# Performance work log

Hardware: AMD Instinct MI355X
Metric: run time of the kernel (lower is better)

Reference implementation:

```python
import jax, jax.numpy as jnp
import numpy as np

D_MODEL = 1024
NUM_HEADS = 16
HEAD_DIM = D_MODEL // NUM_HEADS


def setup_inputs() -> dict:
    key = jax.random.key(0)
    k1, k2, k3 = jax.random.split(key, 3)
    B, T = 4, 2048
    x = jax.random.normal(k1, (B, T, D_MODEL), dtype=jnp.float32)
    # nn.Linear weights: out = x @ W.T; store torch-layout [out_features, in_features]
    w_qkv = jax.random.normal(k2, (3 * D_MODEL, D_MODEL), dtype=jnp.float32) * (D_MODEL ** -0.5)
    w_proj = jax.random.normal(k3, (D_MODEL, D_MODEL), dtype=jnp.float32) * (D_MODEL ** -0.5)
    return {"x": x, "w_qkv": w_qkv, "w_proj": w_proj}


def reference(x, w_qkv, w_proj):
    B, T, C = x.shape
    H, Dh = NUM_HEADS, HEAD_DIM
    qkv = jnp.einsum('btc,fc->btf', x, w_qkv)          # [B,T,3C]
    q, k, v = jnp.split(qkv, 3, axis=2)
    # [B,T,C] -> [B,H,T,Dh]
    q = q.reshape(B, T, H, Dh).transpose(0, 2, 1, 3)
    k = k.reshape(B, T, H, Dh).transpose(0, 2, 1, 3)
    v = v.reshape(B, T, H, Dh).transpose(0, 2, 1, 3)
    scale = Dh ** -0.5
    att = jnp.einsum('bhqd,bhkd->bhqk', q, k) * scale  # [B,H,T,T]
    causal = jnp.tril(jnp.ones((T, T), dtype=bool))
    att = jnp.where(causal, att, -jnp.inf)
    att = jax.nn.softmax(att, axis=-1)
    y = jnp.einsum('bhqk,bhkd->bhqd', att, v)          # [B,H,T,Dh]
    y = y.transpose(0, 2, 1, 3).reshape(B, T, C)
    return jnp.einsum('btc,oc->bto', y, w_proj)
```

## Files before the change

### kernel.cpp

```cpp
#include <hip/hip_runtime.h>
#include <stdint.h>
#include <math.h>

typedef __bf16 bf16;
typedef __bf16 bf16x4 __attribute__((ext_vector_type(4)));
typedef __bf16 bf16x8 __attribute__((ext_vector_type(8)));
typedef float f32x4 __attribute__((ext_vector_type(4)));

#define MFMA16(a, b, c) __builtin_amdgcn_mfma_f32_16x16x32_bf16((a), (b), (c), 0, 0, 0)

typedef __attribute__((address_space(1))) void* as1v;
typedef __attribute__((address_space(3))) void* as3v;

__device__ __forceinline__ void async_ld16(const void* g, void* l) {
  __builtin_amdgcn_global_load_lds((as1v)(uintptr_t)g,
                                   (as3v)(unsigned int)(uintptr_t)l, 16, 0, 0);
}

__global__ __launch_bounds__(256) void cast3_k(const float* __restrict__ x,
                                               const float* __restrict__ wq,
                                               const float* __restrict__ wp,
                                               bf16* __restrict__ xb,
                                               bf16* __restrict__ wqb,
                                               bf16* __restrict__ wpb) {
  const long i = (long)blockIdx.x * 256 + threadIdx.x;
  const float4* src;
  bf16x4* dst;
  long off;
  if (i < 2097152L) {
    src = (const float4*)x;  dst = (bf16x4*)xb;  off = i;
  } else if (i < 2097152L + 786432L) {
    src = (const float4*)wq; dst = (bf16x4*)wqb; off = i - 2097152L;
  } else {
    src = (const float4*)wp; dst = (bf16x4*)wpb; off = i - 2097152L - 786432L;
  }
  float4 v = src[off];
  bf16x4 o;
  o[0] = (bf16)v.x; o[1] = (bf16)v.y; o[2] = (bf16)v.z; o[3] = (bf16)v.w;
  dst[off] = o;
}

__global__ __launch_bounds__(256, 2) void gemm_qkv(const bf16* __restrict__ A,
                                                   const bf16* __restrict__ Bm,
                                                   bf16* __restrict__ qb,
                                                   bf16* __restrict__ kb,
                                                   bf16* __restrict__ vth) {
  __shared__ bf16 As[2][128 * 64];
  __shared__ bf16 Bs[2][192 * 64];
  const int tid  = threadIdx.x;
  const int lane = tid & 63;
  const int wv   = tid >> 6;
  const int wm   = wv >> 1;
  const int wn   = wv & 1;
  const int lr   = lane & 15;
  const int quad = lane >> 4;
  const long m0 = (long)blockIdx.y * 128;
  const long n0 = (long)blockIdx.x * 192;

  const int srow = lane >> 3;
  const int scg  = (lane & 7) ^ srow;
  const int swz  = lr & 7;

  const f32x4 fz = {0.f, 0.f, 0.f, 0.f};
  f32x4 acc[4][6];
#pragma unroll
  for (int i = 0; i < 4; ++i)
#pragma unroll
    for (int j = 0; j < 6; ++j) acc[i][j] = fz;

#define STAGE_QKV(kt, bufi)                                                        \
  do {                                                                             \
    const long kk = (long)(kt) * 64;                                               \
    _Pragma("unroll") for (int i_ = 0; i_ < 4; ++i_)                               \
        async_ld16(&A[(m0 + i_ * 32 + wv * 8 + srow) * 1024 + kk + scg * 8],       \
                   &As[bufi][(i_ * 32 + wv * 8) * 64]);                            \
    _Pragma("unroll") for (int i_ = 0; i_ < 6; ++i_)                               \
        async_ld16(&Bm[(n0 + i_ * 32 + wv * 8 + srow) * 1024 + kk + scg * 8],      \
                   &Bs[bufi][(i_ * 32 + wv * 8) * 64]);                            \
  } while (0)

  STAGE_QKV(0, 0);

#pragma unroll 2
  for (int t = 0; t < 16; ++t) {
    const int cur = t & 1;
    if (t < 15) {
      STAGE_QKV(t + 1, cur ^ 1);
      asm volatile("s_waitcnt vmcnt(10)" ::: "memory");
    } else {
      asm volatile("s_waitcnt vmcnt(0)" ::: "memory");
    }
    __builtin_amdgcn_s_barrier();

    bf16x8 af[2][4], bfr[2][6];
#pragma unroll
    for (int ds = 0; ds < 2; ++ds) {
      const int slot = ((ds << 2) + quad) ^ swz;
#pragma unroll
      for (int mi = 0; mi < 4; ++mi)
        af[ds][mi] = *(const bf16x8*)&As[cur][(wm * 64 + mi * 16 + lr) * 64 + slot * 8];
#pragma unroll
      for (int ni = 0; ni < 6; ++ni)
        bfr[ds][ni] = *(const bf16x8*)&Bs[cur][(wn * 96 + ni * 16 + lr) * 64 + slot * 8];
    }
#pragma unroll
    for (int ds = 0; ds < 2; ++ds)
#pragma unroll
      for (int mi = 0; mi < 4; ++mi)
#pragma unroll
        for (int ni = 0; ni < 6; ++ni)
          acc[mi][ni] = MFMA16(af[ds][mi], bfr[ds][ni], acc[mi][ni]);

    if (t < 15) __builtin_amdgcn_s_barrier();
  }
#undef STAGE_QKV

  const float kS = 0.18033688f;
#pragma unroll
  for (int mi = 0; mi < 4; ++mi) {
    const long row = m0 + wm * 64 + mi * 16 + quad * 4;
#pragma unroll
    for (int ni = 0; ni < 6; ++ni) {
      const long col = n0 + wn * 96 + ni * 16 + lr;
      if (col < 1024) {
#pragma unroll
        for (int r = 0; r < 4; ++r) qb[(row + r) * 1024 + col] = (bf16)(acc[mi][ni][r] * kS);
      } else if (col < 2048) {
        const long kc = col - 1024;
#pragma unroll
        for (int r = 0; r < 4; ++r) kb[(row + r) * 1024 + kc] = (bf16)(acc[mi][ni][r]);
      } else {
        const long vcol = col - 2048;
        const long h = vcol >> 6, d = vcol & 63;
        const long b = row >> 11;
        const long tt = row & 2047;
        bf16x4 pk;
#pragma unroll
        for (int r = 0; r < 4; ++r) pk[r] = (bf16)(acc[mi][ni][r]);
        *(bf16x4*)&vth[(((b << 4) + h) * 64 + d) * 2048 + tt] = pk;
      }
    }
  }
}

__global__ __launch_bounds__(128, 2) void gemm_proj(const bf16* __restrict__ A,
                                                    const bf16* __restrict__ Bm,
                                                    float* __restrict__ C) {
  __shared__ bf16 As[128 * 64];
  __shared__ bf16 Bs[128 * 64];
  const int tid  = threadIdx.x;
  const int lane = tid & 63;
  const int wv   = tid >> 6;
  const int lr   = lane & 15;
  const int quad = lane >> 4;
  const long m0 = (long)blockIdx.y * 128;
  const long n0 = (long)blockIdx.x * 128;

  const int srow = lane >> 3;
  const int scg  = (lane & 7) ^ srow;
  const int swz  = lr & 7;

  const f32x4 fz = {0.f, 0.f, 0.f, 0.f};
  f32x4 acc[4][8];
#pragma unroll
  for (int i = 0; i < 4; ++i)
#pragma unroll
    for (int j = 0; j < 8; ++j) acc[i][j] = fz;

  for (int k0 = 0; k0 < 1024; k0 += 64) {
    __syncthreads();
#pragma unroll
    for (int i = 0; i < 8; ++i) {
      const int rb = wv * 64 + i * 8;
      async_ld16(&A[(m0 + rb + srow) * 1024 + k0 + scg * 8], &As[rb * 64]);
      async_ld16(&Bm[(n0 + rb + srow) * 1024 + k0 + scg * 8], &Bs[rb * 64]);
    }
    __syncthreads();

#pragma unroll
    for (int ds = 0; ds < 2; ++ds) {
      const int slot = ((ds << 2) + quad) ^ swz;
      bf16x8 af[4], bfr[8];
#pragma unroll
      for (int mi = 0; mi < 4; ++mi)
        af[mi] = *(const bf16x8*)&As[(wv * 64 + mi * 16 + lr) * 64 + slot * 8];
#pragma unroll
      for (int ni = 0; ni < 8; ++ni)
        bfr[ni] = *(const bf16x8*)&Bs[(ni * 16 + lr) * 64 + slot * 8];
#pragma unroll
      for (int mi = 0; mi < 4; ++mi)
#pragma unroll
        for (int ni = 0; ni < 8; ++ni)
          acc[mi][ni] = MFMA16(af[mi], bfr[ni], acc[mi][ni]);
    }
  }

#pragma unroll
  for (int mi = 0; mi < 4; ++mi) {
    const long row = m0 + wv * 64 + mi * 16 + quad * 4;
#pragma unroll
    for (int ni = 0; ni < 8; ++ni) {
      const long col = n0 + ni * 16 + lr;
#pragma unroll
      for (int r = 0; r < 4; ++r) C[(row + r) * 1024 + col] = acc[mi][ni][r];
    }
  }
}

__global__ __launch_bounds__(256, 2) void flash_attn5(const bf16* __restrict__ q,
                                                      const bf16* __restrict__ k,
                                                      const bf16* __restrict__ vth,
                                                      bf16* __restrict__ y) {
  __shared__ bf16 Ks[2][64 * 64];
  __shared__ bf16 Vt[64 * 64];
  __shared__ bf16 Ps[4][32 * 72];
  const int tid  = threadIdx.x;
  const int lane = tid & 63;
  const int wv   = tid >> 6;
  const int lr   = lane & 15;
  const int quad = lane >> 4;
  const int p  = blockIdx.x;
  const int bh = blockIdx.y;
  const int b = bh >> 4, h = bh & 15;
  const bf16* qp = q + ((size_t)b * 2048) * 1024 + h * 64;
  const bf16* kp = k + ((size_t)b * 2048) * 1024 + h * 64;
  const bf16* vp = vth + (size_t)bh * 64 * 2048;
  bf16* yp = y + ((size_t)b * 2048) * 1024 + h * 64;

  const int stg_row = lane >> 3;
  const int stg_cg  = (lane & 7) ^ stg_row;
  const int swz     = lr & 7;

  bf16x8 ones;
#pragma unroll
  for (int j = 0; j < 8; ++j) ones[j] = (bf16)1.0f;
  const f32x4 fz = {0.f, 0.f, 0.f, 0.f};

  for (int half = 0; half < 2; ++half) {
    const int qt = half ? p : 15 - p;
    const int q0 = qt * 128;
    const int kb_max = 2 * qt + 1;
    const int kmax_w = 2 * qt + (wv >> 1);

    bf16x8 qf[2][2];
#pragma unroll
    for (int nq = 0; nq < 2; ++nq) {
      const int qrow = q0 + wv * 32 + nq * 16 + lr;
#pragma unroll
      for (int ds = 0; ds < 2; ++ds)
        qf[nq][ds] = *(const bf16x8*)(qp + (size_t)qrow * 1024 + ds * 32 + quad * 8);
    }

    f32x4 o[2][4];
    f32x4 lacc[2];
#pragma unroll
    for (int nq = 0; nq < 2; ++nq) {
      lacc[nq] = fz;
#pragma unroll
      for (int nf = 0; nf < 4; ++nf) o[nq][nf] = fz;
    }

    __syncthreads();
#pragma unroll
    for (int i = 0; i < 2; ++i) {
      const int r = i * 32 + wv * 8 + stg_row;
      async_ld16(kp + (size_t)r * 1024 + stg_cg * 8, &Ks[0][(i * 32 + wv * 8) * 64]);
    }

    for (int kt = 0; kt <= kb_max; ++kt) {
      const int k0 = kt * 64;
      const int cb = kt & 1;
      __syncthreads();
      if (kt < kb_max) {
#pragma unroll
        for (int i = 0; i < 2; ++i) {
          const int r = i * 32 + wv * 8 + stg_row;
          async_ld16(kp + (size_t)(k0 + 64 + r) * 1024 + stg_cg * 8,
                     &Ks[cb ^ 1][(i * 32 + wv * 8) * 64]);
        }
      }
#pragma unroll
      for (int i = 0; i < 2; ++i) {
        const int r = i * 32 + wv * 8 + stg_row;
        async_ld16(vp + (size_t)r * 2048 + k0 + stg_cg * 8, &Vt[(i * 32 + wv * 8) * 64]);
      }

      const bool act = (kt <= kmax_w);
      bf16x8 ap[2][2];
      if (act) {
        f32x4 s[2][4];
#pragma unroll
        for (int nq = 0; nq < 2; ++nq)
#pragma unroll
          for (int mi = 0; mi < 4; ++mi) s[nq][mi] = fz;
#pragma unroll
        for (int ds = 0; ds < 2; ++ds)
#pragma unroll
          for (int mi = 0; mi < 4; ++mi) {
            const bf16x8 ak =
                *(const bf16x8*)&Ks[cb][(mi * 16 + lr) * 64 + (((ds << 2) + quad) ^ swz) * 8];
            s[0][mi] = MFMA16(ak, qf[0][ds], s[0][mi]);
            s[1][mi] = MFMA16(ak, qf[1][ds], s[1][mi]);
          }

        if (kt < kmax_w) {
#pragma unroll
          for (int nq = 0; nq < 2; ++nq) {
            const int qloc = nq * 16 + lr;
#pragma unroll
            for (int mi = 0; mi < 4; ++mi) {
              bf16x4 pb;
#pragma unroll
              for (int r = 0; r < 4; ++r) pb[r] = (bf16)__builtin_amdgcn_exp2f(s[nq][mi][r]);
              *(bf16x4*)&Ps[wv][qloc * 72 + mi * 16 + quad * 4] = pb;
            }
          }
        } else {
          const int kofs = k0 - q0 - wv * 32;
#pragma unroll
          for (int nq = 0; nq < 2; ++nq) {
            const int qloc = nq * 16 + lr;
#pragma unroll
            for (int mi = 0; mi < 4; ++mi) {
              bf16x4 pb;
#pragma unroll
              for (int r = 0; r < 4; ++r) {
                float pv = __builtin_amdgcn_exp2f(s[nq][mi][r]);
                if (mi * 16 + quad * 4 + r + kofs > qloc) pv = 0.0f;
                pb[r] = (bf16)pv;
              }
              *(bf16x4*)&Ps[wv][qloc * 72 + mi * 16 + quad * 4] = pb;
            }
          }
        }
#pragma unroll
        for (int ks = 0; ks < 2; ++ks) {
          ap[0][ks] = *(const bf16x8*)&Ps[wv][(lr) * 72 + ks * 32 + quad * 8];
          ap[1][ks] = *(const bf16x8*)&Ps[wv][(16 + lr) * 72 + ks * 32 + quad * 8];
        }
      }

      __syncthreads();

      if (act) {
#pragma unroll
        for (int ks = 0; ks < 2; ++ks) {
          lacc[0] = MFMA16(ap[0][ks], ones, lacc[0]);
          lacc[1] = MFMA16(ap[1][ks], ones, lacc[1]);
#pragma unroll
          for (int nf = 0; nf < 4; ++nf) {
            const bf16x8 bv =
                *(const bf16x8*)&Vt[(nf * 16 + lr) * 64 + (((ks << 2) + quad) ^ swz) * 8];
            o[0][nf] = MFMA16(ap[0][ks], bv, o[0][nf]);
            o[1][nf] = MFMA16(ap[1][ks], bv, o[1][nf]);
          }
        }
      }
    }

#pragma unroll
    for (int nq = 0; nq < 2; ++nq)
#pragma unroll
      for (int r = 0; r < 4; ++r) {
        const float inv = __builtin_amdgcn_rcpf(lacc[nq][r]);
        const int t = q0 + wv * 32 + nq * 16 + quad * 4 + r;
#pragma unroll
        for (int nf = 0; nf < 4; ++nf)
          yp[(size_t)t * 1024 + nf * 16 + lr] = (bf16)(o[nq][nf][r] * inv);
      }
  }
}

extern "C" void kernel_launch(void* const* d_in, const int* in_sizes, int n_in,
                              void* d_out, int out_size, void* d_ws, size_t ws_size,
                              hipStream_t stream) {
  const float* x      = (const float*)d_in[0];
  const float* w_qkv  = (const float*)d_in[1];
  const float* w_proj = (const float*)d_in[2];
  float* out = (float*)d_out;
  char* ws = (char*)d_ws;

  bf16* xb   = (bf16*)(ws);
  bf16* wqkb = (bf16*)(ws + (16ull << 20));
  bf16* wpb  = (bf16*)(ws + (22ull << 20));
  bf16* qb   = (bf16*)(ws + (24ull << 20));
  bf16* kbuf = (bf16*)(ws + (40ull << 20));
  bf16* vth  = (bf16*)(ws + (56ull << 20));
  bf16* yb   = (bf16*)(ws + (72ull << 20));

  cast3_k<<<dim3(12288), 256, 0, stream>>>(x, w_qkv, w_proj, xb, wqkb, wpb);
  gemm_qkv<<<dim3(16, 64), 256, 0, stream>>>(xb, wqkb, qb, kbuf, vth);
  flash_attn5<<<dim3(8, 64), 256, 0, stream>>>(qb, kbuf, vth, yb);
  gemm_proj<<<dim3(8, 64), 128, 0, stream>>>(yb, wpb, out);
}
```

Before: 232.0 us.

## Double-buffer proj GEMM with 4 waves and remap attention blocks per XCD

```diff
diff --git a/kernel.cpp b/kernel.cpp
--- a/kernel.cpp
+++ b/kernel.cpp
@@ -143,14 +143,16 @@
   }
 }
 
-__global__ __launch_bounds__(128, 2) void gemm_proj(const bf16* __restrict__ A,
+__global__ __launch_bounds__(256, 2) void gemm_proj(const bf16* __restrict__ A,
                                                     const bf16* __restrict__ Bm,
                                                     float* __restrict__ C) {
-  __shared__ bf16 As[128 * 64];
-  __shared__ bf16 Bs[128 * 64];
+  __shared__ bf16 As[2][128 * 64];
+  __shared__ bf16 Bs[2][128 * 64];
   const int tid  = threadIdx.x;
   const int lane = tid & 63;
   const int wv   = tid >> 6;
+  const int wm   = wv >> 1;
+  const int wn   = wv & 1;
   const int lr   = lane & 15;
   const int quad = lane >> 4;
   const long m0 = (long)blockIdx.y * 128;
@@ -161,46 +163,64 @@
   const int swz  = lr & 7;
 
   const f32x4 fz = {0.f, 0.f, 0.f, 0.f};
-  f32x4 acc[4][8];
+  f32x4 acc[4][4];
 #pragma unroll
   for (int i = 0; i < 4; ++i)
 #pragma unroll
-    for (int j = 0; j < 8; ++j) acc[i][j] = fz;
-
-  for (int k0 = 0; k0 < 1024; k0 += 64) {
-    __syncthreads();
-#pragma unroll
-    for (int i = 0; i < 8; ++i) {
-      const int rb = wv * 64 + i * 8;
-      async_ld16(&A[(m0 + rb + srow) * 1024 + k0 + scg * 8], &As[rb * 64]);
-      async_ld16(&Bm[(n0 + rb + srow) * 1024 + k0 + scg * 8], &Bs[rb * 64]);
-    }
-    __syncthreads();
-
+    for (int j = 0; j < 4; ++j) acc[i][j] = fz;
+
+#define STAGE_PROJ(kt, bufi)                                                       \
+  do {                                                                             \
+    const long kk = (long)(kt) * 64;                                               \
+    _Pragma("unroll") for (int i_ = 0; i_ < 4; ++i_) {                             \
+      const int rb = i_ * 32 + wv * 8;                                             \
+      async_ld16(&A[(m0 + rb + srow) * 1024 + kk + scg * 8], &As[bufi][rb * 64]);  \
+      async_ld16(&Bm[(n0 + rb + srow) * 1024 + kk + scg * 8], &Bs[bufi][rb * 64]); \
+    }                                                                              \
+  } while (0)
+
+  STAGE_PROJ(0, 0);
+
+#pragma unroll 2
+  for (int t = 0; t < 16; ++t) {
+    const int cur = t & 1;
+    if (t < 15) {
+      STAGE_PROJ(t + 1, cur ^ 1);
+      asm volatile("s_waitcnt vmcnt(8)" ::: "memory");
+    } else {
+      asm volatile("s_waitcnt vmcnt(0)" ::: "memory");
+    }
+    __builtin_amdgcn_s_barrier();
+
+    bf16x8 af[2][4], bfr[2][4];
 #pragma unroll
     for (int ds = 0; ds < 2; ++ds) {
       const int slot = ((ds << 2) + quad) ^ swz;
-      bf16x8 af[4], bfr[8];
 #pragma unroll
       for (int mi = 0; mi < 4; ++mi)
-        af[mi] = *(const bf16x8*)&As[(wv * 64 + mi * 16 + lr) * 64 + slot * 8];
-#pragma unroll
-      for (int ni = 0; ni < 8; ++ni)
-        bfr[ni] = *(const bf16x8*)&Bs[(ni * 16 + lr) * 64 + slot * 8];
+        af[ds][mi] = *(const bf16x8*)&As[cur][(wm * 64 + mi * 16 + lr) * 64 + slot * 8];
+#pragma unroll
+      for (int ni = 0; ni < 4; ++ni)
+        bfr[ds][ni] = *(const bf16x8*)&Bs[cur][(wn * 64 + ni * 16 + lr) * 64 + slot * 8];
+    }
+#pragma unroll
+    for (int ds = 0; ds < 2; ++ds)
 #pragma unroll
       for (int mi = 0; mi < 4; ++mi)
 #pragma unroll
-        for (int ni = 0; ni < 8; ++ni)
-          acc[mi][ni] = MFMA16(af[mi], bfr[ni], acc[mi][ni]);
-    }
-  }
+        for (int ni = 0; ni < 4; ++ni)
+          acc[mi][ni] = MFMA16(af[ds][mi], bfr[ds][ni], acc[mi][ni]);
+
+    if (t < 15) __builtin_amdgcn_s_barrier();
+  }
+#undef STAGE_PROJ
 
 #pragma unroll
   for (int mi = 0; mi < 4; ++mi) {
-    const long row = m0 + wv * 64 + mi * 16 + quad * 4;
-#pragma unroll
-    for (int ni = 0; ni < 8; ++ni) {
-      const long col = n0 + ni * 16 + lr;
+    const long row = m0 + wm * 64 + mi * 16 + quad * 4;
+#pragma unroll
+    for (int ni = 0; ni < 4; ++ni) {
+      const long col = n0 + wn * 64 + ni * 16 + lr;
 #pragma unroll
       for (int r = 0; r < 4; ++r) C[(row + r) * 1024 + col] = acc[mi][ni][r];
     }
@@ -219,8 +239,11 @@
   const int wv   = tid >> 6;
   const int lr   = lane & 15;
   const int quad = lane >> 4;
-  const int p  = blockIdx.x;
-  const int bh = blockIdx.y;
+  const int lin  = blockIdx.x + (blockIdx.y << 3);
+  const int xcd  = lin & 7;
+  const int slot = lin >> 3;
+  const int p    = slot & 7;
+  const int bh   = ((slot >> 3) << 3) | xcd;
   const int b = bh >> 4, h = bh & 15;
   const bf16* qp = q + ((size_t)b * 2048) * 1024 + h * 64;
   const bf16* kp = k + ((size_t)b * 2048) * 1024 + h * 64;
@@ -391,5 +414,5 @@
   cast3_k<<<dim3(12288), 256, 0, stream>>>(x, w_qkv, w_proj, xb, wqkb, wpb);
   gemm_qkv<<<dim3(16, 64), 256, 0, stream>>>(xb, wqkb, qb, kbuf, vth);
   flash_attn5<<<dim3(8, 64), 256, 0, stream>>>(qb, kbuf, vth, yb);
-  gemm_proj<<<dim3(8, 64), 128, 0, stream>>>(yb, wpb, out);
-}
+  gemm_proj<<<dim3(8, 64), 256, 0, stream>>>(yb, wpb, out);
+}
```

Result: faster. 216.6 us (-6.6%).
